# Performance work log

Hardware: AMD Instinct MI355X
Metric: run time of the kernel (lower is better)

Reference implementation:

```python
import jax, jax.numpy as jnp
import numpy as np

B, D, K = 8192, 512, 4096
MAX_WORD_LENGTH = 16
RESIDUAL_THRESHOLD = 0.01
DECAY_FACTOR = 0.95
EPS_TARGET = 1e-8


def setup_inputs() -> dict:
    key = jax.random.key(0)
    k1, k2 = jax.random.split(key)
    targets = jax.random.normal(k1, (B, D), dtype=jnp.float32)
    codebook = jax.random.normal(k2, (K, D), dtype=jnp.float32)
    return {"targets": targets, "codebook": codebook}


def reference(targets, codebook):
    """Batched greedy residual pursuit (allow_negative_signs=True).

    Returns:
      seq      [B, L] int32 signed indices (>=0: add idx; <0: subtract (-idx-1)); 0 where inactive
      mask     [B, L] bool, True where a step actually emitted a symbol
      residual [B, D] final residual after pursuit
    """
    target_norm = jnp.linalg.norm(targets, axis=-1)  # [B]

    def step(residual, step_idx):
        rnorm = jnp.linalg.norm(residual, axis=-1)  # [B]
        active = (rnorm >= RESIDUAL_THRESHOLD) & (target_norm >= EPS_TARGET)
        # cosine similarity of each codebook vector with residual direction
        res_dir = residual / jnp.maximum(rnorm, 1e-12)[:, None]
        cos = jnp.einsum('bd,kd->bk', res_dir, codebook)  # [B, K]
        best = jnp.argmax(jnp.abs(cos), axis=-1)  # [B]
        best_cos = jnp.take_along_axis(cos, best[:, None], axis=-1)[:, 0]
        signed = jnp.where(best_cos >= 0, best, -(best + 1)).astype(jnp.int32)
        sign = jnp.where(best_cos >= 0, 1.0, -1.0).astype(residual.dtype)
        decay = jnp.power(jnp.asarray(DECAY_FACTOR, residual.dtype),
                          (step_idx + 1).astype(residual.dtype))
        contrib = sign[:, None] * decay * codebook[best]  # [B, D]
        new_res = jnp.where(active[:, None], residual - contrib, residual)
        out_idx = jnp.where(active, signed, 0)
        return new_res, (out_idx, active)

    residual, (seq, mask) = jax.lax.scan(step, targets, jnp.arange(MAX_WORD_LENGTH))
    return seq.T, mask.T, residual
```

## Files before the change

### kernel.cpp

```cpp
#include <hip/hip_runtime.h>
#include <hip/hip_bf16.h>

#define B_SZ 8192
#define D_SZ 512
#define K_SZ 4096
#define L_SZ 16
#define M_ALL (B_SZ + K_SZ)

typedef __attribute__((ext_vector_type(8))) short short8v;
typedef __attribute__((ext_vector_type(4))) float f32x4;
typedef _Float16 half8v __attribute__((ext_vector_type(8)));
typedef _Float16 h2 __attribute__((ext_vector_type(2)));
struct H2x4 { h2 a, b, c, d; };

typedef const __attribute__((address_space(1))) void gvoid;
typedef __attribute__((address_space(3))) void lvoid;

static __device__ __forceinline__ h2 habs2(h2 a) {
    unsigned u = __builtin_bit_cast(unsigned, a) & 0x7FFF7FFFu;
    return __builtin_bit_cast(h2, u);
}
static __device__ __forceinline__ h2 hmax2(h2 a, h2 b) {
#if __has_builtin(__builtin_elementwise_max)
    return __builtin_elementwise_max(a, b);
#else
    h2 r; r[0] = a[0] > b[0] ? a[0] : b[0]; r[1] = a[1] > b[1] ? a[1] : b[1]; return r;
#endif
}

__global__ void cast_bf16_kernel(const float* __restrict__ targets,
                                 const float* __restrict__ codebook,
                                 __hip_bfloat16* __restrict__ abf) {
    int idx = blockIdx.x * blockDim.x + threadIdx.x;
    const int total4 = (M_ALL * D_SZ) / 4;
    if (idx >= total4) return;
    int base = idx * 4;
    const float* src = (base < B_SZ * D_SZ) ? (targets + base)
                                            : (codebook + (base - B_SZ * D_SZ));
    float4 v = *(const float4*)src;
    abf[base + 0] = __float2bfloat16(v.x);
    abf[base + 1] = __float2bfloat16(v.y);
    abf[base + 2] = __float2bfloat16(v.z);
    abf[base + 3] = __float2bfloat16(v.w);
}

__global__ void cn2_kernel(const float* __restrict__ codebook,
                           double* __restrict__ cn2) {
    int row  = blockIdx.x * 4 + (threadIdx.x >> 6);
    int lane = threadIdx.x & 63;
    const float* r = codebook + (size_t)row * D_SZ;
    double s = 0.0;
#pragma unroll
    for (int j = 0; j < 8; j++) { double v = (double)r[lane + 64 * j]; s += v * v; }
#pragma unroll
    for (int o = 32; o > 0; o >>= 1) s += __shfl_down(s, o, 64);
    if (lane == 0) cn2[row] = s;
}

#define BM 128
#define BN 128
#define BK 32

__global__ __launch_bounds__(256)
void gemm_bt_kernel(const __hip_bfloat16* __restrict__ A,
                    const __hip_bfloat16* __restrict__ Bm,
                    _Float16* __restrict__ C) {
    __shared__ short As[BM * BK];
    __shared__ short Bs[BN * BK];
    const int tid  = threadIdx.x;
    const int bm   = blockIdx.y * BM;
    const int bn   = blockIdx.x * BN;
    const int wave = tid >> 6, lane = tid & 63;
    const int wm = (wave & 1) * 64, wn = (wave >> 1) * 64;
    const int row16 = lane & 15, quad = lane >> 4;
    const int koff = quad * 8;

    f32x4 acc[4][4] = {};

    const short* Ag = (const short*)A;
    const short* Bg = (const short*)Bm;
    const int srow = lane >> 2;
    const int scol = (lane & 3) * 8;

    for (int k0 = 0; k0 < D_SZ; k0 += BK) {
        __syncthreads();
#pragma unroll
        for (int c = 0; c < 2; c++) {
            int row = (wave * 2 + c) * 16 + srow;
            __builtin_amdgcn_global_load_lds(
                (gvoid*)(Ag + (size_t)(bm + row) * D_SZ + k0 + scol),
                (lvoid*)(As + row * BK + scol), 16, 0, 0);
            __builtin_amdgcn_global_load_lds(
                (gvoid*)(Bg + (size_t)(bn + row) * D_SZ + k0 + scol),
                (lvoid*)(Bs + row * BK + scol), 16, 0, 0);
        }
        __syncthreads();

        short8v af[4], bf[4];
#pragma unroll
        for (int i = 0; i < 4; i++)
            af[i] = *(const short8v*)(As + (wm + i * 16 + row16) * BK + koff);
#pragma unroll
        for (int j = 0; j < 4; j++)
            bf[j] = *(const short8v*)(Bs + (wn + j * 16 + row16) * BK + koff);
#pragma unroll
        for (int i = 0; i < 4; i++)
#pragma unroll
            for (int j = 0; j < 4; j++)
                acc[i][j] = __builtin_amdgcn_mfma_f32_16x16x32_bf16(af[i], bf[j], acc[i][j], 0, 0, 0);
    }

    if (bm < B_SZ) {
#pragma unroll
        for (int i = 0; i < 4; i++) {
            int grow = bm + wm + i * 16 + quad * 4;
#pragma unroll
            for (int j = 0; j < 4; j++) {
                int gcol = bn + wn + j * 16 + row16;
#pragma unroll
                for (int r = 0; r < 4; r++)
                    __builtin_nontemporal_store((_Float16)acc[i][j][r],
                                                &C[(size_t)(grow + r) * K_SZ + gcol]);
            }
        }
    } else {
#pragma unroll
        for (int i = 0; i < 4; i++) {
            int grow = bm + wm + i * 16 + quad * 4;
#pragma unroll
            for (int j = 0; j < 4; j++) {
                int gcol = bn + wn + j * 16 + row16;
#pragma unroll
                for (int r = 0; r < 4; r++)
                    C[(size_t)(grow + r) * K_SZ + gcol] = (_Float16)acc[i][j][r];
            }
        }
    }
}

#define MAXC 16
#define MARGIN 1.5f

__global__ __launch_bounds__(256, 4)
void pursuit_kernel(const float* __restrict__ targets,
                    const float* __restrict__ codebook,
                    const _Float16* __restrict__ S,
                    const double* __restrict__ cn2,
                    float* __restrict__ out) {
    const int wave = threadIdx.x >> 6;
    const int lane = threadIdx.x & 63;
    const int b = blockIdx.x * 4 + wave;
    const int lane8 = lane * 8;

    __shared__ alignas(16) _Float16 g_s[4][K_SZ];
    __shared__ int s_cnt[4];
    __shared__ int s_cand[4][MAXC];
    _Float16* g = g_s[wave];
    int* cnt  = &s_cnt[wave];
    int* cand = s_cand[wave];

    h2 tmax; tmax[0] = (_Float16)0; tmax[1] = (_Float16)0;
    {
        const _Float16* g0 = S + (size_t)b * K_SZ + lane8;
#pragma unroll
        for (int c = 0; c < 8; c++) {
            half8v h = __builtin_nontemporal_load((const half8v*)(g0 + c * 512));
            *(half8v*)&g[c * 512 + lane8] = h;
            H2x4 u = __builtin_bit_cast(H2x4, h);
            tmax = hmax2(tmax, hmax2(hmax2(habs2(u.a), habs2(u.b)),
                                     hmax2(habs2(u.c), habs2(u.d))));
        }
    }
    float m = fmaxf((float)tmax[0], (float)tmax[1]);

    double rres[8];
    double loc = 0.0;
    {
        const float* tg = targets + (size_t)b * D_SZ + lane8;
        f32x4 t0 = __builtin_nontemporal_load((const f32x4*)tg);
        f32x4 t1 = __builtin_nontemporal_load((const f32x4*)(tg + 4));
        rres[0] = t0[0]; rres[1] = t0[1]; rres[2] = t0[2]; rres[3] = t0[3];
        rres[4] = t1[0]; rres[5] = t1[1]; rres[6] = t1[2]; rres[7] = t1[3];
#pragma unroll
        for (int e = 0; e < 8; e++) loc += rres[e] * rres[e];
    }
#pragma unroll
    for (int o = 32; o > 0; o >>= 1) loc += __shfl_xor(loc, o, 64);
    double rn2 = loc;
    const bool tgt_ok = (sqrt(loc) >= 1e-8);

    float* out_seq  = out + (size_t)b * L_SZ;
    float* out_mask = out + (size_t)B_SZ * L_SZ + (size_t)b * L_SZ;
    float* out_res  = out + (size_t)2 * B_SZ * L_SZ + (size_t)b * D_SZ;

    double decay = 1.0;

    for (int t = 0; t < L_SZ; t++) {
        decay *= 0.95;
        bool active = (sqrt(rn2) >= 0.01) && tgt_ok;
        if (!active) {
            if (lane == 0)
                for (int tt = t; tt < L_SZ; tt++) {
                    __builtin_nontemporal_store(0.0f, &out_seq[tt]);
                    __builtin_nontemporal_store(0.0f, &out_mask[tt]);
                }
            break;
        }

        float M = m;
#pragma unroll
        for (int o = 32; o > 0; o >>= 1) M = fmaxf(M, __shfl_xor(M, o, 64));
        float thr = M - MARGIN;

        if (lane == 0) *cnt = 0;
        if (m >= thr) {
#pragma unroll
            for (int c = 0; c < 8; c++) {
                half8v h = *(const half8v*)&g[c * 512 + lane8];
#pragma unroll
                for (int e = 0; e < 8; e++) {
                    float f = fabsf((float)h[e]);
                    if (f >= thr) {
                        int q = atomicAdd(cnt, 1);
                        if (q < MAXC) cand[q] = c * 512 + lane8 + e;
                    }
                }
            }
        }
        __threadfence_block();
        int nc = min(*cnt, MAXC);

        int bk; double bv;
        float4 c0, c1;
        half8v Gh[8];
        if (nc == 1) {
            bk = __builtin_amdgcn_readfirstlane(cand[0]);
            const float* cr = codebook + (size_t)bk * D_SZ + lane8;
            const _Float16* Gp = S + (size_t)(B_SZ + bk) * K_SZ + lane8;
            c0 = *(const float4*)cr;
            c1 = *(const float4*)(cr + 4);
#pragma unroll
            for (int c = 0; c < 8; c++) Gh[c] = *(const half8v*)(Gp + c * 512);
            double s = rres[0] * (double)c0.x + rres[1] * (double)c0.y
                     + rres[2] * (double)c0.z + rres[3] * (double)c0.w
                     + rres[4] * (double)c1.x + rres[5] * (double)c1.y
                     + rres[6] * (double)c1.z + rres[7] * (double)c1.w;
#pragma unroll
            for (int o = 32; o > 0; o >>= 1) s += __shfl_xor(s, o, 64);
            bv = s;
        } else {
            bk = -1; bv = 0.0;
            for (int ci = 0; ci < nc; ci++) {
                int k = __builtin_amdgcn_readfirstlane(cand[ci]);
                const float* cr = codebook + (size_t)k * D_SZ + lane8;
                float4 d0 = *(const float4*)cr;
                float4 d1 = *(const float4*)(cr + 4);
                double s = rres[0] * (double)d0.x + rres[1] * (double)d0.y
                         + rres[2] * (double)d0.z + rres[3] * (double)d0.w
                         + rres[4] * (double)d1.x + rres[5] * (double)d1.y
                         + rres[6] * (double)d1.z + rres[7] * (double)d1.w;
#pragma unroll
                for (int o = 32; o > 0; o >>= 1) s += __shfl_xor(s, o, 64);
                if (bk < 0 || fabs(s) > fabs(bv) ||
                    (fabs(s) == fabs(bv) && k < bk)) { bk = k; bv = s; }
            }
            const float* cr = codebook + (size_t)bk * D_SZ + lane8;
            const _Float16* Gp = S + (size_t)(B_SZ + bk) * K_SZ + lane8;
            c0 = *(const float4*)cr;
            c1 = *(const float4*)(cr + 4);
#pragma unroll
            for (int c = 0; c < 8; c++) Gh[c] = *(const half8v*)(Gp + c * 512);
        }

        const double cn2bk = cn2[bk];
        double sd = ((bv >= 0.0) ? 1.0 : -1.0) * decay;
        rn2 = rn2 - 2.0 * sd * bv + sd * sd * cn2bk;
        if (lane == 0) {
            __builtin_nontemporal_store((float)((bv >= 0.0) ? bk : (-bk - 1)), &out_seq[t]);
            __builtin_nontemporal_store(1.0f, &out_mask[t]);
        }
        const float sdf = (float)sd;
        h2 sdh2; sdh2[0] = (_Float16)sdf; sdh2[1] = (_Float16)sdf;

        tmax[0] = (_Float16)0; tmax[1] = (_Float16)0;
#pragma unroll
        for (int c = 0; c < 8; c++) {
            half8v gv = *(const half8v*)&g[c * 512 + lane8];
            H2x4 ug = __builtin_bit_cast(H2x4, gv);
            H2x4 uG = __builtin_bit_cast(H2x4, Gh[c]);
            ug.a -= sdh2 * uG.a; ug.b -= sdh2 * uG.b;
            ug.c -= sdh2 * uG.c; ug.d -= sdh2 * uG.d;
            *(half8v*)&g[c * 512 + lane8] = __builtin_bit_cast(half8v, ug);
            tmax = hmax2(tmax, hmax2(hmax2(habs2(ug.a), habs2(ug.b)),
                                     hmax2(habs2(ug.c), habs2(ug.d))));
        }
        m = fmaxf((float)tmax[0], (float)tmax[1]);

        if (lane == 0) g[bk] = (_Float16)(float)(bv - sd * cn2bk);

        rres[0] -= sd * (double)c0.x; rres[1] -= sd * (double)c0.y;
        rres[2] -= sd * (double)c0.z; rres[3] -= sd * (double)c0.w;
        rres[4] -= sd * (double)c1.x; rres[5] -= sd * (double)c1.y;
        rres[6] -= sd * (double)c1.z; rres[7] -= sd * (double)c1.w;
    }

    {
        f32x4 r0, r1;
        r0[0] = (float)rres[0]; r0[1] = (float)rres[1]; r0[2] = (float)rres[2]; r0[3] = (float)rres[3];
        r1[0] = (float)rres[4]; r1[1] = (float)rres[5]; r1[2] = (float)rres[6]; r1[3] = (float)rres[7];
        __builtin_nontemporal_store(r0, (f32x4*)(out_res + lane8));
        __builtin_nontemporal_store(r1, (f32x4*)(out_res + lane8 + 4));
    }
}

extern "C" void kernel_launch(void* const* d_in, const int* in_sizes, int n_in,
                              void* d_out, int out_size, void* d_ws, size_t ws_size,
                              hipStream_t stream) {
    const float* targets  = (const float*)d_in[0];
    const float* codebook = (const float*)d_in[1];
    float* out = (float*)d_out;

    __hip_bfloat16* abf = (__hip_bfloat16*)d_ws;
    _Float16* S = (_Float16*)((char*)d_ws + (size_t)M_ALL * D_SZ * 2);
    double* cn2 = (double*)((char*)d_ws + (size_t)M_ALL * D_SZ * 2
                                        + (size_t)M_ALL * K_SZ * 2);

    int total4 = (M_ALL * D_SZ) / 4;
    cast_bf16_kernel<<<(total4 + 255) / 256, 256, 0, stream>>>(targets, codebook, abf);
    cn2_kernel<<<K_SZ / 4, 256, 0, stream>>>(codebook, cn2);

    dim3 ggrid(K_SZ / BN, M_ALL / BM);
    gemm_bt_kernel<<<ggrid, 256, 0, stream>>>(abf, abf + (size_t)B_SZ * D_SZ, S);

    pursuit_kernel<<<B_SZ / 4, 256, 0, stream>>>(targets, codebook, S, cn2, out);
}
```

Before: 335.4 us.

## Interleave two pursuit chains per wave to overlap dependent global loads

Each wavefront now processes two batch rows at once, interleaving their scan, pick, dot and update phases so that the global loads of codebook rows and Gram rows for one chain can overlap with work on the other. The grid is halved, shared memory per block doubles to 8 rows of K halfs, and launch bounds drop to 2 blocks per CU. This aims to hide memory latency through instruction-level parallelism, at the cost of more registers and fewer resident waves, and a chain that terminates early still shares the wave with its partner.

Result: slower. 460.3 us (+37.3%).

```diff
diff --git a/kernel.cpp b/kernel.cpp
--- a/kernel.cpp
+++ b/kernel.cpp
@@ -141,7 +141,160 @@
 #define MAXC 16
 #define MARGIN 1.5f
 
-__global__ __launch_bounds__(256, 4)
+struct Chain {
+    double rres[8];
+    double rn2;
+    float  m;
+    bool   tgt_ok;
+    bool   run;
+    int    b;
+    _Float16* g;
+    int*   cnt;
+    int*   cand;
+};
+
+struct Step {
+    int bk; double bv; bool have_bv;
+    float4 c0, c1;
+    half8v Gh[8];
+};
+
+__device__ __forceinline__ void chain_init(Chain& C, int lane8,
+        const float* __restrict__ targets, const _Float16* __restrict__ S) {
+    h2 tmax; tmax[0] = (_Float16)0; tmax[1] = (_Float16)0;
+    const _Float16* g0 = S + (size_t)C.b * K_SZ + lane8;
+#pragma unroll
+    for (int c = 0; c < 8; c++) {
+        half8v h = __builtin_nontemporal_load((const half8v*)(g0 + c * 512));
+        *(half8v*)&C.g[c * 512 + lane8] = h;
+        H2x4 u = __builtin_bit_cast(H2x4, h);
+        tmax = hmax2(tmax, hmax2(hmax2(habs2(u.a), habs2(u.b)),
+                                 hmax2(habs2(u.c), habs2(u.d))));
+    }
+    C.m = fmaxf((float)tmax[0], (float)tmax[1]);
+
+    const float* tg = targets + (size_t)C.b * D_SZ + lane8;
+    f32x4 t0 = __builtin_nontemporal_load((const f32x4*)tg);
+    f32x4 t1 = __builtin_nontemporal_load((const f32x4*)(tg + 4));
+    C.rres[0] = t0[0]; C.rres[1] = t0[1]; C.rres[2] = t0[2]; C.rres[3] = t0[3];
+    C.rres[4] = t1[0]; C.rres[5] = t1[1]; C.rres[6] = t1[2]; C.rres[7] = t1[3];
+    double loc = 0.0;
+#pragma unroll
+    for (int e = 0; e < 8; e++) loc += C.rres[e] * C.rres[e];
+#pragma unroll
+    for (int o = 32; o > 0; o >>= 1) loc += __shfl_xor(loc, o, 64);
+    C.rn2 = loc;
+    C.tgt_ok = (sqrt(loc) >= 1e-8);
+    C.run = true;
+}
+
+__device__ __forceinline__ void chain_scan(Chain& C, int lane, int lane8) {
+    float M = C.m;
+#pragma unroll
+    for (int o = 32; o > 0; o >>= 1) M = fmaxf(M, __shfl_xor(M, o, 64));
+    float thr = M - MARGIN;
+    if (lane == 0) *C.cnt = 0;
+    if (C.m >= thr) {
+#pragma unroll
+        for (int c = 0; c < 8; c++) {
+            half8v h = *(const half8v*)&C.g[c * 512 + lane8];
+#pragma unroll
+            for (int e = 0; e < 8; e++) {
+                float f = fabsf((float)h[e]);
+                if (f >= thr) {
+                    int q = atomicAdd(C.cnt, 1);
+                    if (q < MAXC) C.cand[q] = c * 512 + lane8 + e;
+                }
+            }
+        }
+    }
+}
+
+__device__ __forceinline__ void chain_pick(Chain& C, Step& st, int nc, int lane8,
+        const float* __restrict__ codebook, const _Float16* __restrict__ S) {
+    if (nc == 1) {
+        st.bk = __builtin_amdgcn_readfirstlane(C.cand[0]);
+        st.have_bv = false;
+        const float* cr = codebook + (size_t)st.bk * D_SZ + lane8;
+        const _Float16* Gp = S + (size_t)(B_SZ + st.bk) * K_SZ + lane8;
+        st.c0 = *(const float4*)cr;
+        st.c1 = *(const float4*)(cr + 4);
+#pragma unroll
+        for (int c = 0; c < 8; c++) st.Gh[c] = *(const half8v*)(Gp + c * 512);
+    } else {
+        int bk = -1; double bv = 0.0;
+        for (int ci = 0; ci < nc; ci++) {
+            int k = __builtin_amdgcn_readfirstlane(C.cand[ci]);
+            const float* cr = codebook + (size_t)k * D_SZ + lane8;
+            float4 d0 = *(const float4*)cr;
+            float4 d1 = *(const float4*)(cr + 4);
+            double s = C.rres[0] * (double)d0.x + C.rres[1] * (double)d0.y
+                     + C.rres[2] * (double)d0.z + C.rres[3] * (double)d0.w
+                     + C.rres[4] * (double)d1.x + C.rres[5] * (double)d1.y
+                     + C.rres[6] * (double)d1.z + C.rres[7] * (double)d1.w;
+#pragma unroll
+            for (int o = 32; o > 0; o >>= 1) s += __shfl_xor(s, o, 64);
+            if (bk < 0 || fabs(s) > fabs(bv) ||
+                (fabs(s) == fabs(bv) && k < bk)) { bk = k; bv = s; }
+        }
+        st.bk = bk; st.bv = bv; st.have_bv = true;
+        const float* cr = codebook + (size_t)bk * D_SZ + lane8;
+        const _Float16* Gp = S + (size_t)(B_SZ + bk) * K_SZ + lane8;
+        st.c0 = *(const float4*)cr;
+        st.c1 = *(const float4*)(cr + 4);
+#pragma unroll
+        for (int c = 0; c < 8; c++) st.Gh[c] = *(const half8v*)(Gp + c * 512);
+    }
+}
+
+__device__ __forceinline__ void chain_dot(Chain& C, Step& st) {
+    if (!st.have_bv) {
+        double s = C.rres[0] * (double)st.c0.x + C.rres[1] * (double)st.c0.y
+                 + C.rres[2] * (double)st.c0.z + C.rres[3] * (double)st.c0.w
+                 + C.rres[4] * (double)st.c1.x + C.rres[5] * (double)st.c1.y
+                 + C.rres[6] * (double)st.c1.z + C.rres[7] * (double)st.c1.w;
+#pragma unroll
+        for (int o = 32; o > 0; o >>= 1) s += __shfl_xor(s, o, 64);
+        st.bv = s;
+    }
+}
+
+__device__ __forceinline__ void chain_finish(Chain& C, Step& st, double decay, int t,
+        int lane, int lane8, const double* __restrict__ cn2,
+        float* out_seq, float* out_mask) {
+    const double cn2bk = cn2[st.bk];
+    double sd = ((st.bv >= 0.0) ? 1.0 : -1.0) * decay;
+    C.rn2 = C.rn2 - 2.0 * sd * st.bv + sd * sd * cn2bk;
+    if (lane == 0) {
+        __builtin_nontemporal_store((float)((st.bv >= 0.0) ? st.bk : (-st.bk - 1)), &out_seq[t]);
+        __builtin_nontemporal_store(1.0f, &out_mask[t]);
+    }
+    const float sdf = (float)sd;
+    h2 sdh2; sdh2[0] = (_Float16)sdf; sdh2[1] = (_Float16)sdf;
+
+    h2 tmax; tmax[0] = (_Float16)0; tmax[1] = (_Float16)0;
+#pragma unroll
+    for (int c = 0; c < 8; c++) {
+        half8v gv = *(const half8v*)&C.g[c * 512 + lane8];
+        H2x4 ug = __builtin_bit_cast(H2x4, gv);
+        H2x4 uG = __builtin_bit_cast(H2x4, st.Gh[c]);
+        ug.a -= sdh2 * uG.a; ug.b -= sdh2 * uG.b;
+        ug.c -= sdh2 * uG.c; ug.d -= sdh2 * uG.d;
+        *(half8v*)&C.g[c * 512 + lane8] = __builtin_bit_cast(half8v, ug);
+        tmax = hmax2(tmax, hmax2(hmax2(habs2(ug.a), habs2(ug.b)),
+                                 hmax2(habs2(ug.c), habs2(ug.d))));
+    }
+    C.m = fmaxf((float)tmax[0], (float)tmax[1]);
+
+    if (lane == 0) C.g[st.bk] = (_Float16)(float)(st.bv - sd * cn2bk);
+
+    C.rres[0] -= sd * (double)st.c0.x; C.rres[1] -= sd * (double)st.c0.y;
+    C.rres[2] -= sd * (double)st.c0.z; C.rres[3] -= sd * (double)st.c0.w;
+    C.rres[4] -= sd * (double)st.c1.x; C.rres[5] -= sd * (double)st.c1.y;
+    C.rres[6] -= sd * (double)st.c1.z; C.rres[7] -= sd * (double)st.c1.w;
+}
+
+__global__ __launch_bounds__(256, 2)
 void pursuit_kernel(const float* __restrict__ targets,
                     const float* __restrict__ codebook,
                     const _Float16* __restrict__ S,
@@ -149,167 +302,82 @@
                     float* __restrict__ out) {
     const int wave = threadIdx.x >> 6;
     const int lane = threadIdx.x & 63;
-    const int b = blockIdx.x * 4 + wave;
     const int lane8 = lane * 8;
 
-    __shared__ alignas(16) _Float16 g_s[4][K_SZ];
-    __shared__ int s_cnt[4];
-    __shared__ int s_cand[4][MAXC];
-    _Float16* g = g_s[wave];
-    int* cnt  = &s_cnt[wave];
-    int* cand = s_cand[wave];
-
-    h2 tmax; tmax[0] = (_Float16)0; tmax[1] = (_Float16)0;
-    {
-        const _Float16* g0 = S + (size_t)b * K_SZ + lane8;
-#pragma unroll
-        for (int c = 0; c < 8; c++) {
-            half8v h = __builtin_nontemporal_load((const half8v*)(g0 + c * 512));
-            *(half8v*)&g[c * 512 + lane8] = h;
-            H2x4 u = __builtin_bit_cast(H2x4, h);
-            tmax = hmax2(tmax, hmax2(hmax2(habs2(u.a), habs2(u.b)),
-                                     hmax2(habs2(u.c), habs2(u.d))));
-        }
-    }
-    float m = fmaxf((float)tmax[0], (float)tmax[1]);
-
-    double rres[8];
-    double loc = 0.0;
-    {
-        const float* tg = targets + (size_t)b * D_SZ + lane8;
-        f32x4 t0 = __builtin_nontemporal_load((const f32x4*)tg);
-        f32x4 t1 = __builtin_nontemporal_load((const f32x4*)(tg + 4));
-        rres[0] = t0[0]; rres[1] = t0[1]; rres[2] = t0[2]; rres[3] = t0[3];
-        rres[4] = t1[0]; rres[5] = t1[1]; rres[6] = t1[2]; rres[7] = t1[3];
-#pragma unroll
-        for (int e = 0; e < 8; e++) loc += rres[e] * rres[e];
-    }
-#pragma unroll
-    for (int o = 32; o > 0; o >>= 1) loc += __shfl_xor(loc, o, 64);
-    double rn2 = loc;
-    const bool tgt_ok = (sqrt(loc) >= 1e-8);
-
-    float* out_seq  = out + (size_t)b * L_SZ;
-    float* out_mask = out + (size_t)B_SZ * L_SZ + (size_t)b * L_SZ;
-    float* out_res  = out + (size_t)2 * B_SZ * L_SZ + (size_t)b * D_SZ;
+    __shared__ alignas(16) _Float16 g_s[8][K_SZ];
+    __shared__ int s_cnt[8];
+    __shared__ int s_cand[8][MAXC];
+
+    Chain A, Bc;
+    A.b  = blockIdx.x * 8 + wave * 2;
+    Bc.b = A.b + 1;
+    A.g  = g_s[wave * 2 + 0];  Bc.g  = g_s[wave * 2 + 1];
+    A.cnt  = &s_cnt[wave * 2 + 0];  Bc.cnt  = &s_cnt[wave * 2 + 1];
+    A.cand = s_cand[wave * 2 + 0];  Bc.cand = s_cand[wave * 2 + 1];
+
+    chain_init(A,  lane8, targets, S);
+    chain_init(Bc, lane8, targets, S);
+
+    float* outA_seq  = out + (size_t)A.b * L_SZ;
+    float* outA_mask = out + (size_t)B_SZ * L_SZ + (size_t)A.b * L_SZ;
+    float* outA_res  = out + (size_t)2 * B_SZ * L_SZ + (size_t)A.b * D_SZ;
+    float* outB_seq  = out + (size_t)Bc.b * L_SZ;
+    float* outB_mask = out + (size_t)B_SZ * L_SZ + (size_t)Bc.b * L_SZ;
+    float* outB_res  = out + (size_t)2 * B_SZ * L_SZ + (size_t)Bc.b * D_SZ;
 
     double decay = 1.0;
 
     for (int t = 0; t < L_SZ; t++) {
         decay *= 0.95;
-        bool active = (sqrt(rn2) >= 0.01) && tgt_ok;
-        if (!active) {
-            if (lane == 0)
-                for (int tt = t; tt < L_SZ; tt++) {
-                    __builtin_nontemporal_store(0.0f, &out_seq[tt]);
-                    __builtin_nontemporal_store(0.0f, &out_mask[tt]);
-                }
-            break;
-        }
-
-        float M = m;
-#pragma unroll
-        for (int o = 32; o > 0; o >>= 1) M = fmaxf(M, __shfl_xor(M, o, 64));
-        float thr = M - MARGIN;
-
-        if (lane == 0) *cnt = 0;
-        if (m >= thr) {
-#pragma unroll
-            for (int c = 0; c < 8; c++) {
-                half8v h = *(const half8v*)&g[c * 512 + lane8];
-#pragma unroll
-                for (int e = 0; e < 8; e++) {
-                    float f = fabsf((float)h[e]);
-                    if (f >= thr) {
-                        int q = atomicAdd(cnt, 1);
-                        if (q < MAXC) cand[q] = c * 512 + lane8 + e;
+        if (A.run) {
+            bool act = (sqrt(A.rn2) >= 0.01) && A.tgt_ok;
+            if (!act) {
+                if (lane == 0)
+                    for (int tt = t; tt < L_SZ; tt++) {
+                        __builtin_nontemporal_store(0.0f, &outA_seq[tt]);
+                        __builtin_nontemporal_store(0.0f, &outA_mask[tt]);
                     }
-                }
+                A.run = false;
             }
         }
+        if (Bc.run) {
+            bool act = (sqrt(Bc.rn2) >= 0.01) && Bc.tgt_ok;
+            if (!act) {
+                if (lane == 0)
+                    for (int tt = t; tt < L_SZ; tt++) {
+                        __builtin_nontemporal_store(0.0f, &outB_seq[tt]);
+                        __builtin_nontemporal_store(0.0f, &outB_mask[tt]);
+                    }
+                Bc.run = false;
+            }
+        }
+        if (!A.run && !Bc.run) break;
+
+        if (A.run)  chain_scan(A,  lane, lane8);
+        if (Bc.run) chain_scan(Bc, lane, lane8);
         __threadfence_block();
-        int nc = min(*cnt, MAXC);
-
-        int bk; double bv;
-        float4 c0, c1;
-        half8v Gh[8];
-        if (nc == 1) {
-            bk = __builtin_amdgcn_readfirstlane(cand[0]);
-            const float* cr = codebook + (size_t)bk * D_SZ + lane8;
-            const _Float16* Gp = S + (size_t)(B_SZ + bk) * K_SZ + lane8;
-            c0 = *(const float4*)cr;
-            c1 = *(const float4*)(cr + 4);
-#pragma unroll
-            for (int c = 0; c < 8; c++) Gh[c] = *(const half8v*)(Gp + c * 512);
-            double s = rres[0] * (double)c0.x + rres[1] * (double)c0.y
-                     + rres[2] * (double)c0.z + rres[3] * (double)c0.w
-                     + rres[4] * (double)c1.x + rres[5] * (double)c1.y
-                     + rres[6] * (double)c1.z + rres[7] * (double)c1.w;
-#pragma unroll
-            for (int o = 32; o > 0; o >>= 1) s += __shfl_xor(s, o, 64);
-            bv = s;
-        } else {
-            bk = -1; bv = 0.0;
-            for (int ci = 0; ci < nc; ci++) {
-                int k = __builtin_amdgcn_readfirstlane(cand[ci]);
-                const float* cr = codebook + (size_t)k * D_SZ + lane8;
-                float4 d0 = *(const float4*)cr;
-                float4 d1 = *(const float4*)(cr + 4);
-                double s = rres[0] * (double)d0.x + rres[1] * (double)d0.y
-                         + rres[2] * (double)d0.z + rres[3] * (double)d0.w
-                         + rres[4] * (double)d1.x + rres[5] * (double)d1.y
-                         + rres[6] * (double)d1.z + rres[7] * (double)d1.w;
-#pragma unroll
-                for (int o = 32; o > 0; o >>= 1) s += __shfl_xor(s, o, 64);
-                if (bk < 0 || fabs(s) > fabs(bv) ||
-                    (fabs(s) == fabs(bv) && k < bk)) { bk = k; bv = s; }
-            }
-            const float* cr = codebook + (size_t)bk * D_SZ + lane8;
-            const _Float16* Gp = S + (size_t)(B_SZ + bk) * K_SZ + lane8;
-            c0 = *(const float4*)cr;
-            c1 = *(const float4*)(cr + 4);
-#pragma unroll
-            for (int c = 0; c < 8; c++) Gh[c] = *(const half8v*)(Gp + c * 512);
-        }
-
-        const double cn2bk = cn2[bk];
-        double sd = ((bv >= 0.0) ? 1.0 : -1.0) * decay;
-        rn2 = rn2 - 2.0 * sd * bv + sd * sd * cn2bk;
-        if (lane == 0) {
-            __builtin_nontemporal_store((float)((bv >= 0.0) ? bk : (-bk - 1)), &out_seq[t]);
-            __builtin_nontemporal_store(1.0f, &out_mask[t]);
-        }
-        const float sdf = (float)sd;
-        h2 sdh2; sdh2[0] = (_Float16)sdf; sdh2[1] = (_Float16)sdf;
-
-        tmax[0] = (_Float16)0; tmax[1] = (_Float16)0;
-#pragma unroll
-        for (int c = 0; c < 8; c++) {
-            half8v gv = *(const half8v*)&g[c * 512 + lane8];
-            H2x4 ug = __builtin_bit_cast(H2x4, gv);
-            H2x4 uG = __builtin_bit_cast(H2x4, Gh[c]);
-            ug.a -= sdh2 * uG.a; ug.b -= sdh2 * uG.b;
-            ug.c -= sdh2 * uG.c; ug.d -= sdh2 * uG.d;
-            *(half8v*)&g[c * 512 + lane8] = __builtin_bit_cast(half8v, ug);
-            tmax = hmax2(tmax, hmax2(hmax2(habs2(ug.a), habs2(ug.b)),
-                                     hmax2(habs2(ug.c), habs2(ug.d))));
-        }
-        m = fmaxf((float)tmax[0], (float)tmax[1]);
-
-        if (lane == 0) g[bk] = (_Float16)(float)(bv - sd * cn2bk);
-
-        rres[0] -= sd * (double)c0.x; rres[1] -= sd * (double)c0.y;
-        rres[2] -= sd * (double)c0.z; rres[3] -= sd * (double)c0.w;
-        rres[4] -= sd * (double)c1.x; rres[5] -= sd * (double)c1.y;
-        rres[6] -= sd * (double)c1.z; rres[7] -= sd * (double)c1.w;
+        int ncA = A.run  ? min(*A.cnt,  MAXC) : 0;
+        int ncB = Bc.run ? min(*Bc.cnt, MAXC) : 0;
+
+        Step sA, sB;
+        if (A.run)  chain_pick(A,  sA, ncA, lane8, codebook, S);
+        if (Bc.run) chain_pick(Bc, sB, ncB, lane8, codebook, S);
+        if (A.run)  chain_dot(A,  sA);
+        if (Bc.run) chain_dot(Bc, sB);
+        if (A.run)  chain_finish(A,  sA, decay, t, lane, lane8, cn2, outA_seq, outA_mask);
+        if (Bc.run) chain_finish(Bc, sB, decay, t, lane, lane8, cn2, outB_seq, outB_mask);
     }
 
     {
         f32x4 r0, r1;
-        r0[0] = (float)rres[0]; r0[1] = (float)rres[1]; r0[2] = (float)rres[2]; r0[3] = (float)rres[3];
-        r1[0] = (float)rres[4]; r1[1] = (float)rres[5]; r1[2] = (float)rres[6]; r1[3] = (float)rres[7];
-        __builtin_nontemporal_store(r0, (f32x4*)(out_res + lane8));
-        __builtin_nontemporal_store(r1, (f32x4*)(out_res + lane8 + 4));
+        r0[0] = (float)A.rres[0]; r0[1] = (float)A.rres[1]; r0[2] = (float)A.rres[2]; r0[3] = (float)A.rres[3];
+        r1[0] = (float)A.rres[4]; r1[1] = (float)A.rres[5]; r1[2] = (float)A.rres[6]; r1[3] = (float)A.rres[7];
+        __builtin_nontemporal_store(r0, (f32x4*)(outA_res + lane8));
+        __builtin_nontemporal_store(r1, (f32x4*)(outA_res + lane8 + 4));
+        r0[0] = (float)Bc.rres[0]; r0[1] = (float)Bc.rres[1]; r0[2] = (float)Bc.rres[2]; r0[3] = (float)Bc.rres[3];
+        r1[0] = (float)Bc.rres[4]; r1[1] = (float)Bc.rres[5]; r1[2] = (float)Bc.rres[6]; r1[3] = (float)Bc.rres[7];
+        __builtin_nontemporal_store(r0, (f32x4*)(outB_res + lane8));
+        __builtin_nontemporal_store(r1, (f32x4*)(outB_res + lane8 + 4));
     }
 }
 
@@ -332,5 +400,5 @@
     dim3 ggrid(K_SZ / BN, M_ALL / BM);
     gemm_bt_kernel<<<ggrid, 256, 0, stream>>>(abf, abf + (size_t)B_SZ * D_SZ, S);
 
-    pursuit_kernel<<<B_SZ / 4, 256, 0, stream>>>(targets, codebook, S, cn2, out);
-}
+    pursuit_kernel<<<B_SZ / 8, 256, 0, stream>>>(targets, codebook, S, cn2, out);
+}
```
